# Kernel tuning notes

Hardware: AMD Instinct MI355X
Metric: run time of the kernel (lower is better)

Reference implementation:

```python
import jax, jax.numpy as jnp
import numpy as np

B, S, E, H = 16, 2048, 128, 128  # batch, seq_len, n_embd, head_dim


def setup_inputs() -> dict:
    key = jax.random.key(0)
    ks = jax.random.split(key, 6)
    init_s = 1.0 / np.sqrt(E)  # ~ torch Linear default init scale
    return {
        "q": jax.random.normal(ks[0], (B, S, E), jnp.float32),
        "k": jax.random.normal(ks[1], (B, S, E), jnp.float32),
        "v": jax.random.normal(ks[2], (B, S, E), jnp.float32),
        "Wq": jax.random.normal(ks[3], (H, E), jnp.float32) * init_s,
        "bq": jnp.zeros((H,), jnp.float32),
        "Wk": jax.random.normal(ks[4], (H, E), jnp.float32) * init_s,
        "bk": jnp.zeros((H,), jnp.float32),
        "Wv": jax.random.normal(ks[5], (H, E), jnp.float32) * init_s,
        "bv": jnp.zeros((H,), jnp.float32),
        "mask": jnp.tril(jnp.ones((S, S), jnp.float32)),  # causal mask
    }


def reference(q, k, v, Wq, bq, Wk, bk, Wv, bv, mask):
    # Linear projections: y = x @ W.T + b (torch nn.Linear convention)
    qh = q @ Wq.T + bq  # [B,S,H]
    kh = k @ Wk.T + bk  # [B,S,H]
    vh = v @ Wv.T + bv  # [B,S,H]
    d_k = kh.shape[-1]
    wei = jnp.einsum("bqd,bkd->bqk", qh, kh) * (d_k ** -0.5)  # [B,S,S]
    wei = jnp.where(mask == 0, -jnp.inf, wei)  # masked_fill(mask==0, -inf)
    attn = jax.nn.softmax(wei, axis=-1)
    return jnp.einsum("bqk,bkd->bqd", attn, vh)  # [B,S,H]
```

## Files before the change

### kernel.cpp

```cpp
#include <hip/hip_runtime.h>
#include <hip/hip_bf16.h>

#define BATCH 16
#define SEQ   2048
#define HD    128
#define TB    64
#define QB2   128
#define KB2   128
#define NTB   (SEQ/KB2)
#define PLANE ((size_t)BATCH*SEQ*HD)

typedef __attribute__((ext_vector_type(8)))  short bf16x8;
typedef __attribute__((ext_vector_type(4)))  float f32x4;
typedef __attribute__((ext_vector_type(16))) float f32x16;

#define MFMA(a,b,c)   __builtin_amdgcn_mfma_f32_16x16x32_bf16(a,b,c,0,0,0)
#define MFMA32(a,b,c) __builtin_amdgcn_mfma_f32_32x32x16_bf16(a,b,c,0,0,0)

__device__ __forceinline__ short f2bf(float f){
  union{float f; unsigned u;} v; v.f = f;
  unsigned r = (v.u + 0x7FFFu + ((v.u>>16)&1u))>>16;
  return (short)r;
}
__device__ __forceinline__ unsigned packbf(float lo, float hi){
  return ((unsigned)(unsigned short)f2bf(hi) << 16) | (unsigned short)f2bf(lo);
}
__device__ __forceinline__ bf16x8 pack8(f32x4 a, f32x4 b){
  bf16x8 r;
  r[0]=f2bf(a[0]); r[1]=f2bf(a[1]); r[2]=f2bf(a[2]); r[3]=f2bf(a[3]);
  r[4]=f2bf(b[0]); r[5]=f2bf(b[1]); r[6]=f2bf(b[2]); r[7]=f2bf(b[3]);
  return r;
}
__device__ __forceinline__ bf16x8 ldfrag(const float* base, size_t eo){
  const float* p = base + eo;
  return pack8(*(const f32x4*)p, *(const f32x4*)(p+4));
}
__device__ __forceinline__ bf16x8 mkfrag(unsigned w0, unsigned w1,
                                         unsigned w2, unsigned w3){
  union{ unsigned u[4]; bf16x8 v; } t;
  t.u[0]=w0; t.u[1]=w1; t.u[2]=w2; t.u[3]=w3;
  return t.v;
}

__global__ __launch_bounds__(256)
void wconv_kernel(const float* __restrict__ Wq, const float* __restrict__ Wk,
                  const float* __restrict__ Wv, short* __restrict__ wb)
{
  int i = (blockIdx.x*256 + threadIdx.x)*8;
  const float* src = (i < 16384) ? Wq : (i < 32768 ? Wk : Wv);
  int off = i & 16383;
  f32x4 a = *(const f32x4*)(src + off);
  f32x4 b = *(const f32x4*)(src + off + 4);
  *(bf16x8*)(wb + i) = pack8(a, b);
}

__global__ __launch_bounds__(256)
void proj_kernel(const float* __restrict__ q, const float* __restrict__ k,
                 const float* __restrict__ v,
                 const float* __restrict__ bq, const float* __restrict__ bk,
                 const float* __restrict__ bv,
                 const short* __restrict__ wb, short* __restrict__ ws)
{
  __shared__ __align__(16) short T[TB*136];
  __shared__ __align__(16) short VT[HD*72];

  const int z = blockIdx.y;
  const float* x  = z==0 ? q  : (z==1 ? k  : v);
  const float* bb = z==0 ? bq : (z==1 ? bk : bv);
  const short* W  = wb + (size_t)z*HD*HD;

  const int tid = threadIdx.x;
  const int w = tid>>6, l = tid&63, li = l&15, g = l>>4;
  const int bx = blockIdx.x;
  const int rowbase = bx*TB + w*16;

  bf16x8 afr[4];
  const float* xr = x + (size_t)(rowbase+li)*HD + g*8;
  #pragma unroll
  for (int ks=0; ks<4; ks++) afr[ks] = ldfrag(xr, (size_t)ks*32);

  f32x4 acc[8];
  #pragma unroll
  for (int ct=0; ct<8; ct++) acc[ct] = (f32x4){0.f,0.f,0.f,0.f};
  #pragma unroll
  for (int ct=0; ct<8; ct++){
    #pragma unroll
    for (int ks=0; ks<4; ks++){
      bf16x8 bfr = *(const bf16x8*)(W + (size_t)(ct*16+li)*HD + ks*32 + g*8);
      acc[ct] = MFMA(afr[ks], bfr, acc[ct]);
    }
  }

  const int img  = (bx>>1);
  const int half = bx & 1;

  if (z < 2){
    #pragma unroll
    for (int ct=0; ct<8; ct++){
      float bias = bb[ct*16+li];
      #pragma unroll
      for (int r=0; r<4; r++)
        T[(w*16+g*4+r)*136 + ct*16+li] = f2bf(acc[ct][r] + bias);
    }
    __syncthreads();
    if (z == 0){
      short* dst = ws + (size_t)bx*TB*HD;
      #pragma unroll
      for (int it=0; it<4; it++){
        int c = tid + it*256, row = c>>4, c8 = c&15;
        *(bf16x8*)(dst + row*HD + c8*8) = *(const bf16x8*)&T[row*136 + c8*8];
      }
    } else {
      short* dst = ws + PLANE + (size_t)img*16384;
      #pragma unroll
      for (int it=0; it<4; it++){
        int c = tid + it*256, row = c>>4, c8 = c&15;
        int r128 = half*64 + row;
        int chunk = r128*16 + (c8 ^ (r128&7));
        *(bf16x8*)(dst + chunk*8) = *(const bf16x8*)&T[row*136 + c8*8];
      }
    }
  } else {
    #pragma unroll
    for (int ct=0; ct<8; ct++){
      float bias = bb[ct*16+li];
      #pragma unroll
      for (int r=0; r<4; r++)
        VT[(ct*16+li)*72 + w*16+g*4+r] = f2bf(acc[ct][r] + bias);
    }
    __syncthreads();
    short* dst = ws + 2*PLANE + (size_t)img*16384;
    const int d = tid>>1, hf = tid&1;
    #pragma unroll
    for (int j=0; j<4; j++){
      int c8l = hf*4 + j;
      int c8g = half*8 + c8l;
      int chunk = d*16 + (c8g ^ (d&7));
      *(bf16x8*)(dst + chunk*8) = *(const bf16x8*)&VT[d*72 + c8l*8];
    }
  }
}

__global__ __launch_bounds__(512, 2)
void attn_kernel(const short* __restrict__ ws, float* __restrict__ out)
{
  __shared__ __align__(16) short KVL[2][32768];
  __shared__ float sm[4][2][2][32];
  __shared__ float scl_l[4][2][32];

  const int bid  = blockIdx.x;
  const int xcd  = bid & 7, slot = bid >> 3;
  const int b    = xcd*2 + (slot >> 4);
  const int qt   = slot & 15;

  const int tid = threadIdx.x;
  const int w = tid>>6, l = tid&63;
  const int s = w & 3, h = w >> 2;
  const int lq = l & 31, h5 = l >> 5;

  const short* Qw    = ws;
  const short* KimgB = ws + PLANE   + (size_t)b*NTB*16384;
  const short* VimgB = ws + 2*PLANE + (size_t)b*NTB*16384;

  const size_t qbase = (size_t)b*SEQ + qt*QB2;
  const float sc = 0.088388347648318447f;
  const int qg = (int)(qt*QB2) + s*32 + lq;

  bf16x8 qfr[8];
  #pragma unroll
  for (int ks=0; ks<8; ks++)
    qfr[ks] = *(const bf16x8*)&Qw[(qbase + s*32 + lq)*HD + ks*16 + h5*8];

  f32x16 oacc[4];
  #pragma unroll
  for (int db=0; db<4; db++) oacc[db] = (f32x16)(0.f);
  float m_run = -1e30f, l_run = 0.f;

  bf16x8 stg[8];
  #define LOADT(kt_) do{                                                    \
    const short* sK = KimgB + (size_t)(kt_)*16384;                          \
    const short* sV = VimgB + (size_t)(kt_)*16384;                          \
    _Pragma("unroll")                                                       \
    for (int j=0;j<4;j++) stg[j]   = *(const bf16x8*)(sK + (tid + j*512)*8);\
    _Pragma("unroll")                                                       \
    for (int j=0;j<4;j++) stg[4+j] = *(const bf16x8*)(sV + (tid + j*512)*8);\
  }while(0)
  #define WRT(nb_) do{                                                     \
    short* dK = &KVL[nb_][0];                                              \
    short* dV = &KVL[nb_][16384];                                          \
    _Pragma("unroll")                                                      \
    for (int j=0;j<4;j++) *(bf16x8*)(dK + (tid+j*512)*8) = stg[j];         \
    _Pragma("unroll")                                                      \
    for (int j=0;j<4;j++) *(bf16x8*)(dV + (tid+j*512)*8) = stg[4+j];       \
  }while(0)

  LOADT(0); WRT(0); __syncthreads();
  int cur = 0;

  for (int kt=0; kt<=qt; kt++){
    const bool pre = (kt < qt);
    if (pre) LOADT(kt+1);

    const short* KL = &KVL[cur][0];
    const short* VL = &KVL[cur][16384];

    f32x16 sacc[2];
    sacc[0] = (f32x16)(0.f); sacc[1] = (f32x16)(0.f);
    #pragma unroll
    for (int ct=0; ct<2; ct++){
      const int r = h*64 + ct*32 + lq;
      #pragma unroll
      for (int ks=0; ks<8; ks++){
        const int chunk = r*16 + ((2*ks + h5) ^ (r&7));
        bf16x8 kfr = *(const bf16x8*)&KL[chunk*8];
        sacc[ct] = MFMA32(kfr, qfr[ks], sacc[ct]);
      }
    }

    float sv[2][16];
    float pm = -1e30f;
    const bool diag = (kt == qt);
    #pragma unroll
    for (int ct=0; ct<2; ct++){
      #pragma unroll
      for (int r=0; r<16; r++){
        float x = sacc[ct][r]*sc;
        if (diag){
          int k_loc = h*64 + ct*32 + (r&3) + 8*(r>>2) + 4*h5;
          if (kt*KB2 + k_loc > qg - (int)(qt*QB2) + (int)(qt*KB2)) x = -1e30f;
        }
        sv[ct][r] = x;
        pm = fmaxf(pm, x);
      }
    }
    pm = fmaxf(pm, __shfl_xor(pm, 32));
    float psum = 0.f;
    #pragma unroll
    for (int ct=0; ct<2; ct++){
      #pragma unroll
      for (int r=0; r<16; r++){
        float p = __expf(sv[ct][r] - pm);
        sv[ct][r] = p;
        psum += p;
      }
    }
    psum += __shfl_xor(psum, 32);

    if (l < 32){ sm[s][h][0][lq] = pm; sm[s][h][1][lq] = psum; }
    __syncthreads();
    float pm_p = sm[s][h^1][0][lq];
    float ps_p = sm[s][h^1][1][lq];
    float m_new  = fmaxf(m_run, fmaxf(pm, pm_p));
    float sclq   = __expf(m_run - m_new);
    float pscale = __expf(pm - m_new);
    m_run = m_new;
    l_run = l_run*sclq + psum*pscale;
    (void)ps_p;
    if (l < 32) scl_l[s][h][lq] = sclq;

    float sclr[16];
    #pragma unroll
    for (int r=0; r<16; r++)
      sclr[r] = scl_l[s][h][(r&3) + 8*(r>>2) + 4*h5];
    #pragma unroll
    for (int db=0; db<4; db++){
      #pragma unroll
      for (int r=0; r<16; r++) oacc[db][r] *= sclr[r];
    }

    #pragma unroll
    for (int ct=0; ct<2; ct++){
      unsigned G[4][2], GX[4][2];
      #pragma unroll
      for (int g2=0; g2<4; g2++){
        #pragma unroll
        for (int p=0; p<2; p++)
          G[g2][p] = packbf(sv[ct][g2*4+2*p]*pscale, sv[ct][g2*4+2*p+1]*pscale);
      }
      #pragma unroll
      for (int g2=0; g2<4; g2++){
        #pragma unroll
        for (int p=0; p<2; p++)
          GX[g2][p] = __shfl_xor((int)G[g2][p], 32);
      }
      bf16x8 pf0 = h5 ? mkfrag(GX[1][0],GX[1][1],G[1][0],G[1][1])
                      : mkfrag(G[0][0],G[0][1],GX[0][0],GX[0][1]);
      bf16x8 pf1 = h5 ? mkfrag(GX[3][0],GX[3][1],G[3][0],G[3][1])
                      : mkfrag(G[2][0],G[2][1],GX[2][0],GX[2][1]);
      #pragma unroll
      for (int ksp=0; ksp<2; ksp++){
        bf16x8 pf = ksp ? pf1 : pf0;
        #pragma unroll
        for (int db=0; db<4; db++){
          const int d = db*32 + lq;
          const int c8 = h*8 + ct*4 + ksp*2 + h5;
          const int chunk = d*16 + (c8 ^ (d&7));
          bf16x8 vfr = *(const bf16x8*)&VL[chunk*8];
          oacc[db] = MFMA32(pf, vfr, oacc[db]);
        }
      }
    }

    if (pre) WRT(cur^1);
    __syncthreads();
    cur ^= 1;
  }

  if (l < 32) sm[s][h][1][lq] = l_run;
  float* Obuf = (float*)&KVL[0][0];
  if (h == 1){
    #pragma unroll
    for (int db=0; db<4; db++){
      #pragma unroll
      for (int r=0; r<16; r++){
        int qr = (r&3) + 8*(r>>2) + 4*h5;
        Obuf[s*4096 + qr*128 + db*32 + lq] = oacc[db][r];
      }
    }
  }
  __syncthreads();
  if (h == 0){
    float lt[16];
    #pragma unroll
    for (int r=0; r<16; r++){
      int qr = (r&3) + 8*(r>>2) + 4*h5;
      lt[r] = sm[s][0][1][qr] + sm[s][1][1][qr];
    }
    #pragma unroll
    for (int db=0; db<4; db++){
      #pragma unroll
      for (int r=0; r<16; r++){
        int qr = (r&3) + 8*(r>>2) + 4*h5;
        float o = (oacc[db][r] + Obuf[s*4096 + qr*128 + db*32 + lq]) / lt[r];
        out[(qbase + s*32 + qr)*HD + db*32 + lq] = o;
      }
    }
  }
  #undef LOADT
  #undef WRT
}

extern "C" void kernel_launch(void* const* d_in, const int* in_sizes, int n_in,
                              void* d_out, int out_size, void* d_ws, size_t ws_size,
                              hipStream_t stream)
{
  short* ws = (short*)d_ws;
  short* wb = ws + 3*PLANE;

  wconv_kernel<<<24, 256, 0, stream>>>(
      (const float*)d_in[3], (const float*)d_in[5], (const float*)d_in[7], wb);

  dim3 pg(BATCH*SEQ/TB, 3);
  proj_kernel<<<pg, 256, 0, stream>>>(
      (const float*)d_in[0], (const float*)d_in[1], (const float*)d_in[2],
      (const float*)d_in[4], (const float*)d_in[6], (const float*)d_in[8],
      wb, ws);

  attn_kernel<<<dim3(BATCH*NTB), 512, 0, stream>>>(ws, (float*)d_out);
}
```

Before: 108.0 us.

## Keep independent per-half softmax state and merge halves once at the end

Each key-half wave group now keeps its own running max and sum, so the per-tile shared-memory exchange and the extra __syncthreads inside the loop go away. The two halves are merged with a rescale step in the epilogue. The per-row rescale factor is broadcast with __shfl instead of a shared-memory round trip. s_setprio hints are added around the MFMA sections. The cost is a heavier epilogue with more exp calls and shuffles per element.

```diff
diff --git a/kernel.cpp b/kernel.cpp
--- a/kernel.cpp
+++ b/kernel.cpp
@@ -146,7 +146,6 @@
 {
   __shared__ __align__(16) short KVL[2][32768];
   __shared__ float sm[4][2][2][32];
-  __shared__ float scl_l[4][2][32];
 
   const int bid  = blockIdx.x;
   const int xcd  = bid & 7, slot = bid >> 3;
@@ -164,7 +163,7 @@
 
   const size_t qbase = (size_t)b*SEQ + qt*QB2;
   const float sc = 0.088388347648318447f;
-  const int qg = (int)(qt*QB2) + s*32 + lq;
+  const int qloc = s*32 + lq;
 
   bf16x8 qfr[8];
   #pragma unroll
@@ -206,6 +205,7 @@
 
     f32x16 sacc[2];
     sacc[0] = (f32x16)(0.f); sacc[1] = (f32x16)(0.f);
+    __builtin_amdgcn_s_setprio(1);
     #pragma unroll
     for (int ct=0; ct<2; ct++){
       const int r = h*64 + ct*32 + lq;
@@ -216,6 +216,7 @@
         sacc[ct] = MFMA32(kfr, qfr[ks], sacc[ct]);
       }
     }
+    __builtin_amdgcn_s_setprio(0);
 
     float sv[2][16];
     float pm = -1e30f;
@@ -227,47 +228,39 @@
         float x = sacc[ct][r]*sc;
         if (diag){
           int k_loc = h*64 + ct*32 + (r&3) + 8*(r>>2) + 4*h5;
-          if (kt*KB2 + k_loc > qg - (int)(qt*QB2) + (int)(qt*KB2)) x = -1e30f;
+          if (k_loc > qloc) x = -1e30f;
         }
         sv[ct][r] = x;
         pm = fmaxf(pm, x);
       }
     }
     pm = fmaxf(pm, __shfl_xor(pm, 32));
+    float m_new = fmaxf(m_run, pm);
+    float sclq  = __expf(m_run - m_new);
+    m_run = m_new;
     float psum = 0.f;
     #pragma unroll
     for (int ct=0; ct<2; ct++){
       #pragma unroll
       for (int r=0; r<16; r++){
-        float p = __expf(sv[ct][r] - pm);
+        float p = __expf(sv[ct][r] - m_new);
         sv[ct][r] = p;
         psum += p;
       }
     }
     psum += __shfl_xor(psum, 32);
-
-    if (l < 32){ sm[s][h][0][lq] = pm; sm[s][h][1][lq] = psum; }
-    __syncthreads();
-    float pm_p = sm[s][h^1][0][lq];
-    float ps_p = sm[s][h^1][1][lq];
-    float m_new  = fmaxf(m_run, fmaxf(pm, pm_p));
-    float sclq   = __expf(m_run - m_new);
-    float pscale = __expf(pm - m_new);
-    m_run = m_new;
-    l_run = l_run*sclq + psum*pscale;
-    (void)ps_p;
-    if (l < 32) scl_l[s][h][lq] = sclq;
-
-    float sclr[16];
-    #pragma unroll
-    for (int r=0; r<16; r++)
-      sclr[r] = scl_l[s][h][(r&3) + 8*(r>>2) + 4*h5];
+    l_run = l_run*sclq + psum;
+
     #pragma unroll
     for (int db=0; db<4; db++){
       #pragma unroll
-      for (int r=0; r<16; r++) oacc[db][r] *= sclr[r];
-    }
-
+      for (int r=0; r<16; r++){
+        float f = __shfl(sclq, (r&3) + 8*(r>>2) + 4*h5);
+        oacc[db][r] *= f;
+      }
+    }
+
+    __builtin_amdgcn_s_setprio(1);
     #pragma unroll
     for (int ct=0; ct<2; ct++){
       unsigned G[4][2], GX[4][2];
@@ -275,7 +268,7 @@
       for (int g2=0; g2<4; g2++){
         #pragma unroll
         for (int p=0; p<2; p++)
-          G[g2][p] = packbf(sv[ct][g2*4+2*p]*pscale, sv[ct][g2*4+2*p+1]*pscale);
+          G[g2][p] = packbf(sv[ct][g2*4+2*p], sv[ct][g2*4+2*p+1]);
       }
       #pragma unroll
       for (int g2=0; g2<4; g2++){
@@ -300,13 +293,19 @@
         }
       }
     }
+    __builtin_amdgcn_s_setprio(0);
 
     if (pre) WRT(cur^1);
     __syncthreads();
     cur ^= 1;
   }
 
-  if (l < 32) sm[s][h][1][lq] = l_run;
+  if (l < 32){ sm[s][h][0][lq] = m_run; sm[s][h][1][lq] = l_run; }
+  __syncthreads();
+  float m_p = sm[s][h^1][0][lq];
+  float M   = fmaxf(m_run, m_p);
+  float sfac = __expf(m_run - M);
+
   float* Obuf = (float*)&KVL[0][0];
   if (h == 1){
     #pragma unroll
@@ -314,24 +313,24 @@
       #pragma unroll
       for (int r=0; r<16; r++){
         int qr = (r&3) + 8*(r>>2) + 4*h5;
-        Obuf[s*4096 + qr*128 + db*32 + lq] = oacc[db][r];
+        float fw = __shfl(sfac, qr);
+        Obuf[s*4096 + qr*128 + db*32 + lq] = oacc[db][r]*fw;
       }
     }
   }
   __syncthreads();
   if (h == 0){
-    float lt[16];
-    #pragma unroll
-    for (int r=0; r<16; r++){
-      int qr = (r&3) + 8*(r>>2) + 4*h5;
-      lt[r] = sm[s][0][1][qr] + sm[s][1][1][qr];
-    }
     #pragma unroll
     for (int db=0; db<4; db++){
       #pragma unroll
       for (int r=0; r<16; r++){
         int qr = (r&3) + 8*(r>>2) + 4*h5;
-        float o = (oacc[db][r] + Obuf[s*4096 + qr*128 + db*32 + lq]) / lt[r];
+        float m0 = sm[s][0][0][qr], l0 = sm[s][0][1][qr];
+        float m1 = sm[s][1][0][qr], l1 = sm[s][1][1][qr];
+        float Mq = fmaxf(m0, m1);
+        float lt = l0*__expf(m0-Mq) + l1*__expf(m1-Mq);
+        float fw = __shfl(sfac, qr);
+        float o = (oacc[db][r]*fw + Obuf[s*4096 + qr*128 + db*32 + lq]) / lt;
         out[(qbase + s*32 + qr)*HD + db*32 + lq] = o;
       }
     }
```

New measurement: 111.1 us. 1.03x slower.
